# Optimization experiments

Hardware: AMD Instinct MI355X
Metric: run time of the kernel (lower is better)

The kernel has to match this reference:

```python
import jax, jax.numpy as jnp
import numpy as np

TEMPERATURE = 0.1
NORMALIZE = True
EPS = 1e-8  # matches torch F.normalize eps-free clamp behavior closely enough for randn inputs

B, D = 4096, 512


def setup_inputs() -> dict:
    key = jax.random.key(0)
    k1, k2 = jax.random.split(key)
    z_i = jax.random.normal(k1, (B, D), dtype=jnp.float32)
    z_j = jax.random.normal(k2, (B, D), dtype=jnp.float32)
    return {"z_i": z_i, "z_j": z_j}


def _l2_normalize(x):
    # torch.F.normalize: x / max(||x||, eps)
    n = jnp.linalg.norm(x, axis=1, keepdims=True)
    return x / jnp.maximum(n, 1e-12)


def reference(z_i, z_j):
    b = z_i.shape[0]
    if NORMALIZE:
        z_i = _l2_normalize(z_i)
        z_j = _l2_normalize(z_j)
    z = jnp.concatenate([z_i, z_j], axis=0)               # (2B, D)
    logits = (z @ z.T) / TEMPERATURE                      # (2B, 2B)
    n = 2 * b
    diag = jnp.eye(n, dtype=bool)
    logits = jnp.where(diag, -jnp.inf, logits)
    row = jnp.arange(n)
    pos_col = (row + b) % n
    pos_logits = logits[row, pos_col]                     # (2B,)
    lse = jax.scipy.special.logsumexp(logits, axis=1)     # stable logsumexp per row
    loss = -(pos_logits - lse).mean()
    return loss
```

## Files before the change

kernel.cpp:

```cpp
#include <hip/hip_runtime.h>
#include <stdint.h>

#define D_DIM 512
#define B_ROWS 4096
#define N_ROWS 8192
#define SCALE_L2E 14.426950408889634f

#define NHP 8
#define NBLK 8256

typedef __attribute__((ext_vector_type(4))) float f32x4;
typedef __attribute__((ext_vector_type(2))) long f8x16;

__global__ __launch_bounds__(256) void k_normalize(const float* __restrict__ zi,
                                                   const float* __restrict__ zj,
                                                   unsigned char* __restrict__ Zn,
                                                   float* __restrict__ pos) {
    const int t = threadIdx.x;
    const int lane = t & 63;
    const int i = blockIdx.x * 4 + (t >> 6);
    const float* pa = zi + (size_t)i * D_DIM + lane * 8;
    const float* pb = zj + (size_t)i * D_DIM + lane * 8;
    const float4 a0 = *(const float4*)pa;
    const float4 a1 = *(const float4*)(pa + 4);
    const float4 b0 = *(const float4*)pb;
    const float4 b1 = *(const float4*)(pb + 4);
    float ssi = a0.x*a0.x + a0.y*a0.y + a0.z*a0.z + a0.w*a0.w
              + a1.x*a1.x + a1.y*a1.y + a1.z*a1.z + a1.w*a1.w;
    float ssj = b0.x*b0.x + b0.y*b0.y + b0.z*b0.z + b0.w*b0.w
              + b1.x*b1.x + b1.y*b1.y + b1.z*b1.z + b1.w*b1.w;
    float dt  = a0.x*b0.x + a0.y*b0.y + a0.z*b0.z + a0.w*b0.w
              + a1.x*b1.x + a1.y*b1.y + a1.z*b1.z + a1.w*b1.w;
    #pragma unroll
    for (int off = 1; off < 64; off <<= 1) {
        ssi += __shfl_xor(ssi, off);
        ssj += __shfl_xor(ssj, off);
        dt  += __shfl_xor(dt,  off);
    }
    const float si = 1.0f / fmaxf(sqrtf(ssi), 1e-12f);
    const float sj = 1.0f / fmaxf(sqrtf(ssj), 1e-12f);
    uint2 pi8, pj8;
    {
        int w0 = 0, w1 = 0;
        w0 = __builtin_amdgcn_cvt_pk_fp8_f32(a0.x * si, a0.y * si, w0, false);
        w0 = __builtin_amdgcn_cvt_pk_fp8_f32(a0.z * si, a0.w * si, w0, true);
        w1 = __builtin_amdgcn_cvt_pk_fp8_f32(a1.x * si, a1.y * si, w1, false);
        w1 = __builtin_amdgcn_cvt_pk_fp8_f32(a1.z * si, a1.w * si, w1, true);
        pi8.x = (unsigned)w0; pi8.y = (unsigned)w1;
        w0 = 0; w1 = 0;
        w0 = __builtin_amdgcn_cvt_pk_fp8_f32(b0.x * sj, b0.y * sj, w0, false);
        w0 = __builtin_amdgcn_cvt_pk_fp8_f32(b0.z * sj, b0.w * sj, w0, true);
        w1 = __builtin_amdgcn_cvt_pk_fp8_f32(b1.x * sj, b1.y * sj, w1, false);
        w1 = __builtin_amdgcn_cvt_pk_fp8_f32(b1.z * sj, b1.w * sj, w1, true);
        pj8.x = (unsigned)w0; pj8.y = (unsigned)w1;
    }
    const size_t PLANE = (size_t)N_ROWS * 64;
    const int o = lane & 7;
    const size_t off0 = (size_t)(lane >> 3) * PLANE + (o & 3) * 16 + (o >> 2) * 8;
    *(uint2*)(Zn + off0 + (size_t)i * 64) = pi8;
    *(uint2*)(Zn + off0 + (size_t)(B_ROWS + i) * 64) = pj8;
    if (lane == 0) pos[i] = 20.0f * dt * si * sj;
}

__global__ __launch_bounds__(64, 4) void k_gemm_lse(const unsigned char* __restrict__ Zn,
                                                    float* __restrict__ rowsum_g) {
    const int lane = threadIdx.x & 63;
    const int l15  = lane & 15, lhi = lane >> 4;

    int g = (blockIdx.x & 7) * (NBLK / 8) + (blockIdx.x >> 3);
    int SI = 0, SJ = 0;
    {
        bool found = false;
        for (SI = 0; SI < 8 && !found; ++SI) {
            for (SJ = SI; SJ < 8; ++SJ) {
                const int sz = (SI == SJ) ? 136 : 256;
                if (g < sz) { found = true; break; }
                g -= sz;
            }
        }
        --SI;
    }
    int di, dj;
    if (SI == SJ) {
        di = 0;
        while (g >= 16 - di) { g -= 16 - di; ++di; }
        dj = di + g;
    } else {
        di = g >> 4; dj = g & 15;
    }
    const int I = SI * 16 + di, J = SJ * 16 + dj;
    const bool dg = (I == J);
    const int rowB = I * 64;
    const int colB = J * 64;

    const char* Zb = (const char*)Zn;
    const size_t PLANE = (size_t)N_ROWS * 64;

    const char* pA = Zb + ((size_t)(rowB + l15)) * 64 + lhi * 16;
    const char* pB = Zb + ((size_t)(colB + l15)) * 64 + lhi * 16;

    f32x4 acc[4][4];
    #pragma unroll
    for (int a = 0; a < 4; ++a)
        #pragma unroll
        for (int b = 0; b < 4; ++b)
            #pragma unroll
            for (int q = 0; q < 4; ++q) acc[a][b][q] = 0.0f;

    for (int hp = 0; hp < NHP; ++hp) {
        f8x16 af[4], bg[4];
        const char* _a = pA + (size_t)hp * PLANE;
        const char* _b = pB + (size_t)hp * PLANE;
        #pragma unroll
        for (int mi = 0; mi < 4; ++mi) af[mi] = *(const f8x16*)(_a + mi * 1024);
        #pragma unroll
        for (int ni = 0; ni < 4; ++ni) bg[ni] = *(const f8x16*)(_b + ni * 1024);
        __builtin_amdgcn_s_setprio(1);
        #pragma unroll
        for (int mi = 0; mi < 4; ++mi)
            #pragma unroll
            for (int ni = 0; ni < 4; ++ni)
                acc[mi][ni] = __builtin_amdgcn_mfma_f32_16x16x32_fp8_fp8(
                    af[mi][0], bg[ni][0], acc[mi][ni], 0, 0, 0);
        #pragma unroll
        for (int mi = 0; mi < 4; ++mi)
            #pragma unroll
            for (int ni = 0; ni < 4; ++ni)
                acc[mi][ni] = __builtin_amdgcn_mfma_f32_16x16x32_fp8_fp8(
                    af[mi][1], bg[ni][1], acc[mi][ni], 0, 0, 0);
        __builtin_amdgcn_s_setprio(0);
    }

    float colsum[4] = {0.0f, 0.0f, 0.0f, 0.0f};
    #pragma unroll
    for (int mi = 0; mi < 4; ++mi) {
        const int growb = rowB + mi * 16 + lhi * 4;
        float rs[4] = {0.0f, 0.0f, 0.0f, 0.0f};
        if (dg) {
            #pragma unroll
            for (int ni = 0; ni < 4; ++ni) {
                const int gcol = colB + ni * 16 + l15;
                #pragma unroll
                for (int r = 0; r < 4; ++r) {
                    float arg = acc[mi][ni][r] * SCALE_L2E;
                    if (growb + r == gcol) arg = -1e30f;
                    rs[r] += exp2f(arg);
                }
            }
        } else {
            #pragma unroll
            for (int ni = 0; ni < 4; ++ni)
                #pragma unroll
                for (int r = 0; r < 4; ++r) {
                    const float e = exp2f(acc[mi][ni][r] * SCALE_L2E);
                    rs[r] += e;
                    colsum[ni] += e;
                }
        }
        #pragma unroll
        for (int r = 0; r < 4; ++r) {
            float v = rs[r];
            v += __shfl_xor(v, 1);
            v += __shfl_xor(v, 2);
            v += __shfl_xor(v, 4);
            v += __shfl_xor(v, 8);
            if (l15 == 0) atomicAdd(&rowsum_g[growb + r], v);
        }
    }
    if (!dg) {
        #pragma unroll
        for (int ni = 0; ni < 4; ++ni) {
            float c = colsum[ni];
            c += __shfl_xor(c, 16);
            c += __shfl_xor(c, 32);
            if (lhi == 0)
                atomicAdd(&rowsum_g[colB + ni * 16 + l15], c);
        }
    }
}

__global__ __launch_bounds__(1024) void k_finalize(const float* __restrict__ rowsum_g,
                                                   const float* __restrict__ pos,
                                                   float* __restrict__ out) {
    const int t = threadIdx.x;
    float l = 0.0f, p = 0.0f;
    #pragma unroll
    for (int q = 0; q < N_ROWS / 1024; ++q) l += logf(rowsum_g[t + q * 1024]);
    #pragma unroll
    for (int q = 0; q < B_ROWS / 1024; ++q) p += pos[t + q * 1024];
    #pragma unroll
    for (int off = 1; off < 64; off <<= 1) {
        l += __shfl_xor(l, off);
        p += __shfl_xor(p, off);
    }
    __shared__ float red[2][16];
    if ((t & 63) == 0) { red[0][t >> 6] = l; red[1][t >> 6] = p; }
    __syncthreads();
    if (t == 0) {
        float L = 0.0f, P = 0.0f;
        #pragma unroll
        for (int q = 0; q < 16; ++q) { L += red[0][q]; P += red[1][q]; }
        out[0] = (L - P) * (1.0f / (float)N_ROWS);
    }
}

extern "C" void kernel_launch(void* const* d_in, const int* in_sizes, int n_in,
                              void* d_out, int out_size, void* d_ws, size_t ws_size,
                              hipStream_t stream) {
    (void)in_sizes; (void)n_in; (void)out_size; (void)ws_size;
    const float* zi = (const float*)d_in[0];
    const float* zj = (const float*)d_in[1];

    const size_t ZN_BYTES = (size_t)N_ROWS * D_DIM;
    unsigned char* Zn     = (unsigned char*)d_ws;
    float* rowsum_g       = (float*)((char*)d_ws + ZN_BYTES);
    float* pos            = (float*)((char*)d_ws + ZN_BYTES + N_ROWS * 4);

    hipMemsetAsync(rowsum_g, 0, N_ROWS * 4, stream);

    k_normalize<<<B_ROWS / 4, 256, 0, stream>>>(zi, zj, Zn, pos);
    k_gemm_lse<<<NBLK, 64, 0, stream>>>(Zn, rowsum_g);
    k_finalize<<<1, 1024, 0, stream>>>(rowsum_g, pos, (float*)d_out);
}
```

Before: 60.67 us.

## Use 16x16x128 scaled fp8 MFMA with 128-byte K-plane layout

Switches the GEMM inner loop from 16x16x32 fp8 MFMA to the gfx950 scaled 16x16x128 f8f6f4 MFMA with unit scales (0x7F). The normalize kernel's fp8 output layout changes to 128-byte K planes so each lane loads 32 contiguous bytes per fragment. The A fragments are now double-buffered one row block ahead of use to overlap their loads with the MFMAs. This cuts the MFMA instruction count and the number of K iterations, at the cost of larger per-load register footprints and possible register pressure at 4 waves/SIMD.

Result: slower. 185.7 us (+206.1%).

```diff
diff --git a/kernel.cpp b/kernel.cpp
--- a/kernel.cpp
+++ b/kernel.cpp
@@ -6,11 +6,12 @@
 #define N_ROWS 8192
 #define SCALE_L2E 14.426950408889634f
 
-#define NHP 8
+#define NKB 4
 #define NBLK 8256
 
 typedef __attribute__((ext_vector_type(4))) float f32x4;
-typedef __attribute__((ext_vector_type(2))) long f8x16;
+typedef __attribute__((ext_vector_type(8))) int i32x8;
+#define SCALE1 0x7F7F7F7F
 
 __global__ __launch_bounds__(256) void k_normalize(const float* __restrict__ zi,
                                                    const float* __restrict__ zj,
@@ -54,11 +55,10 @@
         w1 = __builtin_amdgcn_cvt_pk_fp8_f32(b1.z * sj, b1.w * sj, w1, true);
         pj8.x = (unsigned)w0; pj8.y = (unsigned)w1;
     }
-    const size_t PLANE = (size_t)N_ROWS * 64;
-    const int o = lane & 7;
-    const size_t off0 = (size_t)(lane >> 3) * PLANE + (o & 3) * 16 + (o >> 2) * 8;
-    *(uint2*)(Zn + off0 + (size_t)i * 64) = pi8;
-    *(uint2*)(Zn + off0 + (size_t)(B_ROWS + i) * 64) = pj8;
+    const size_t PLANE = (size_t)N_ROWS * 128;
+    const size_t off0 = (size_t)(lane >> 4) * PLANE + (lane & 15) * 8;
+    *(uint2*)(Zn + off0 + (size_t)i * 128) = pi8;
+    *(uint2*)(Zn + off0 + (size_t)(B_ROWS + i) * 128) = pj8;
     if (lane == 0) pos[i] = 20.0f * dt * si * sj;
 }
 
@@ -94,10 +94,10 @@
     const int colB = J * 64;
 
     const char* Zb = (const char*)Zn;
-    const size_t PLANE = (size_t)N_ROWS * 64;
-
-    const char* pA = Zb + ((size_t)(rowB + l15)) * 64 + lhi * 16;
-    const char* pB = Zb + ((size_t)(colB + l15)) * 64 + lhi * 16;
+    const size_t PLANE = (size_t)N_ROWS * 128;
+
+    const char* pA = Zb + ((size_t)(rowB + l15)) * 128 + lhi * 32;
+    const char* pB = Zb + ((size_t)(colB + l15)) * 128 + lhi * 32;
 
     f32x4 acc[4][4];
     #pragma unroll
@@ -107,28 +107,27 @@
             #pragma unroll
             for (int q = 0; q < 4; ++q) acc[a][b][q] = 0.0f;
 
-    for (int hp = 0; hp < NHP; ++hp) {
-        f8x16 af[4], bg[4];
-        const char* _a = pA + (size_t)hp * PLANE;
-        const char* _b = pB + (size_t)hp * PLANE;
-        #pragma unroll
-        for (int mi = 0; mi < 4; ++mi) af[mi] = *(const f8x16*)(_a + mi * 1024);
-        #pragma unroll
-        for (int ni = 0; ni < 4; ++ni) bg[ni] = *(const f8x16*)(_b + ni * 1024);
-        __builtin_amdgcn_s_setprio(1);
-        #pragma unroll
-        for (int mi = 0; mi < 4; ++mi)
+    #pragma unroll
+    for (int kb = 0; kb < NKB; ++kb) {
+        const char* _a = pA + (size_t)kb * PLANE;
+        const char* _b = pB + (size_t)kb * PLANE;
+        i32x8 bg[4];
+        #pragma unroll
+        for (int ni = 0; ni < 4; ++ni) bg[ni] = *(const i32x8*)(_b + ni * 2048);
+        i32x8 af[2];
+        af[0] = *(const i32x8*)(_a);
+        #pragma unroll
+        for (int mi = 0; mi < 4; ++mi) {
+            if (mi < 3) af[(mi + 1) & 1] = *(const i32x8*)(_a + (mi + 1) * 2048);
+            __builtin_amdgcn_s_setprio(1);
             #pragma unroll
             for (int ni = 0; ni < 4; ++ni)
-                acc[mi][ni] = __builtin_amdgcn_mfma_f32_16x16x32_fp8_fp8(
-                    af[mi][0], bg[ni][0], acc[mi][ni], 0, 0, 0);
-        #pragma unroll
-        for (int mi = 0; mi < 4; ++mi)
-            #pragma unroll
-            for (int ni = 0; ni < 4; ++ni)
-                acc[mi][ni] = __builtin_amdgcn_mfma_f32_16x16x32_fp8_fp8(
-                    af[mi][1], bg[ni][1], acc[mi][ni], 0, 0, 0);
-        __builtin_amdgcn_s_setprio(0);
+                acc[mi][ni] = __builtin_amdgcn_mfma_scale_f32_16x16x128_f8f6f4(
+                    af[mi & 1], bg[ni], acc[mi][ni],
+                    0 , 0 ,
+                    0, SCALE1, 0, SCALE1);
+            __builtin_amdgcn_s_setprio(0);
+        }
     }
 
     float colsum[4] = {0.0f, 0.0f, 0.0f, 0.0f};
```
